# Kernel tuning notes

Hardware: AMD Instinct MI355X
Metric: run time of the kernel (lower is better)

Reference implementation:

```python
import jax, jax.numpy as jnp
import numpy as np

CAPACITY = 0.125


def setup_inputs() -> dict:
    key = jax.random.key(0)
    ks = jax.random.split(key, 6)
    b, s, d, dff = 4, 8192, 512, 2048
    x = jax.random.normal(ks[0], (b, s, d), dtype=jnp.float32)
    position_ids = jnp.tile(jnp.arange(s, dtype=jnp.int64)[None, :], (b, 1))
    Wr = jax.random.normal(ks[1], (d,), dtype=jnp.float32) * 0.02
    br = jnp.zeros((1,), dtype=jnp.float32)
    W1 = jax.random.normal(ks[2], (d, dff), dtype=jnp.float32) * 0.02
    b1 = jnp.zeros((dff,), dtype=jnp.float32)
    W2 = jax.random.normal(ks[3], (dff, d), dtype=jnp.float32) * 0.02
    b2 = jnp.zeros((d,), dtype=jnp.float32)
    return {"x": x, "position_ids": position_ids, "Wr": Wr, "br": br,
            "W1": W1, "b1": b1, "W2": W2, "b2": b2}


def reference(x, position_ids, Wr, br, W1, b1, W2, b2):
    b, s, d = x.shape
    # Router: Linear(d, 1) -> squeeze(-1)
    weights = jnp.einsum('bsd,d->bs', x, Wr) + br  # [b, s]
    k = int(CAPACITY * s)
    # Per-batch top-k threshold (k-th largest value)
    top_k_values = jax.lax.top_k(weights, k)[0]  # [b, k], sorted desc
    threshold = top_k_values[:, -1]              # [b]
    selected_mask = weights > threshold[:, None]  # strict >, ties excluded (matches torch)
    # Block: per-token MLP (Linear-GELU-Linear). Per-token ops commute with the
    # gather/scatter, so computing densely and masking is mathematically identical
    # to the original gather -> block -> weighted scatter.
    h = jax.nn.gelu(jnp.einsum('bsd,df->bsf', x, W1) + b1)
    y = jnp.einsum('bsf,fd->bsd', h, W2) + b2
    # processed_tokens (= block_out * router_weight on selected) + x on unselected
    out = jnp.where(selected_mask[..., None], y * weights[..., None], x)
    return out
```

## Files before the change

### kernel.cpp

```cpp
#include <hip/hip_runtime.h>
#include <hip/hip_bf16.h>

#define B_   4
#define S_   8192
#define D_   512
#define DFF_ 2048
#define K_TOP 1024
#define KS1  8
#define KS2  32
#define TILE_E (128*64)

typedef unsigned short u16;
typedef __attribute__((ext_vector_type(8))) short bf16x8;
typedef __attribute__((ext_vector_type(4))) float floatx4;

__device__ __forceinline__ unsigned f2key(float f){
    unsigned u = __float_as_uint(f);
    return (u & 0x80000000u) ? ~u : (u | 0x80000000u);
}
__device__ __forceinline__ u16 f2b(float f){
    unsigned u = __float_as_uint(f);
    u = (u + 0x7FFFu + ((u >> 16) & 1u)) >> 16;
    return (u16)u;
}
__device__ __forceinline__ float gelu_tanh(float v){
    float c = 0.7978845608028654f * (v + 0.044715f * v * v * v);
    return 0.5f * v * (1.0f + tanhf(c));
}
__device__ __forceinline__ void gl_lds16(const void* gptr, void* lptr){
    auto g = (const __attribute__((address_space(1))) unsigned int*)((uintptr_t)gptr);
    auto l = (__attribute__((address_space(3))) unsigned int*)((uintptr_t)lptr);
    __builtin_amdgcn_global_load_lds(g, l, 16, 0, 0);
}


__global__ __launch_bounds__(256) void wts_copy_kernel(
    const float4* __restrict__ x, float4* __restrict__ out,
    const float4* __restrict__ Wr4, const float* __restrict__ br,
    float* __restrict__ w_all, int* __restrict__ count)
{
    if (blockIdx.x == 0 && threadIdx.x == 0) *count = 0;
    const int wv = threadIdx.x >> 6, lane = threadIdx.x & 63;
    const int token = blockIdx.x * 4 + wv;
    const float4* xt = x + (size_t)token * 128;
    float acc = 0.f;
    #pragma unroll
    for (int i = 0; i < 2; i++){
        int j = lane + i * 64;
        float4 v = xt[j];
        out[(size_t)token * 128 + j] = v;
        float4 wvv = Wr4[j];
        acc += v.x*wvv.x + v.y*wvv.y + v.z*wvv.z + v.w*wvv.w;
    }
    #pragma unroll
    for (int off = 32; off > 0; off >>= 1) acc += __shfl_down(acc, off, 64);
    if (lane == 0) w_all[token] = acc + br[0];
}

__global__ __launch_bounds__(1024) void kth_compact_kernel(
    const float4* __restrict__ w_all4, int* __restrict__ count,
    int* __restrict__ idx)
{
    __shared__ unsigned keys[S_];
    __shared__ unsigned hist[16][256];
    __shared__ unsigned suffix[256];
    __shared__ unsigned sprefix;
    __shared__ int sremk;
    const int b = blockIdx.x, tid = threadIdx.x, wv = tid >> 6;
    const float4* row4 = w_all4 + (size_t)b * (S_ / 4);

    #pragma unroll
    for (int i = 0; i < 2; i++){
        int j = tid + i * 1024;
        float4 v = row4[j];
        keys[4*j+0] = f2key(v.x); keys[4*j+1] = f2key(v.y);
        keys[4*j+2] = f2key(v.z); keys[4*j+3] = f2key(v.w);
    }
    if (tid == 0){ sprefix = 0u; sremk = K_TOP; }
    __syncthreads();

    for (int pass = 3; pass >= 0; pass--){
        for (int i = tid; i < 16 * 256; i += 1024) ((unsigned*)hist)[i] = 0u;
        __syncthreads();
        const unsigned mask_hi = (pass == 3) ? 0u : (0xFFFFFFFFu << ((pass + 1) * 8));
        const unsigned pfx = sprefix;
        const int shift = pass * 8;
        #pragma unroll
        for (int i = 0; i < 8; i++){
            unsigned key = keys[tid + i * 1024];
            if ((key & mask_hi) == pfx)
                atomicAdd(&hist[wv][(key >> shift) & 255u], 1u);
        }
        __syncthreads();
        if (tid < 256){
            unsigned s = 0;
            #pragma unroll
            for (int h = 0; h < 16; h++) s += hist[h][tid];
            suffix[tid] = s;
        }
        __syncthreads();
        for (int off = 1; off < 256; off <<= 1){
            unsigned v = 0;
            if (tid < 256 && tid + off < 256) v = suffix[tid + off];
            __syncthreads();
            if (tid < 256) suffix[tid] += v;
            __syncthreads();
        }
        const int remk = sremk;
        __syncthreads();
        if (tid < 256){
            unsigned snext = (tid == 255) ? 0u : suffix[tid + 1];
            if (suffix[tid] >= (unsigned)remk && snext < (unsigned)remk){
                sprefix = pfx | ((unsigned)tid << shift);
                sremk = remk - (int)snext;
            }
        }
        __syncthreads();
    }

    const unsigned thr = sprefix;
    #pragma unroll
    for (int i = 0; i < 8; i++){
        int li = tid + i * 1024;
        if (keys[li] > thr){
            int p = atomicAdd(count, 1);
            idx[p] = b * S_ + li;
        }
    }
}

__global__ __launch_bounds__(256) void gather_kernel(
    const float* __restrict__ x, const int* __restrict__ idx,
    const int* __restrict__ countp, u16* __restrict__ XbT)
{
    const int mt = blockIdx.x, s = blockIdx.y;
    const int cnt = *countp;
    const int cl = threadIdx.x & 7, rb = threadIdx.x >> 3;
    #pragma unroll
    for (int it = 0; it < 4; it++){
        int r = rb + it * 32;
        int mg = mt * 128 + r;
        if (mg < cnt){
            const float* xp = x + (size_t)idx[mg] * D_ + s * 64 + cl * 8;
            float4 v0 = *(const float4*)xp;
            float4 v1 = *(const float4*)(xp + 4);
            bf16x8 bv;
            bv[0]=(short)f2b(v0.x); bv[1]=(short)f2b(v0.y);
            bv[2]=(short)f2b(v0.z); bv[3]=(short)f2b(v0.w);
            bv[4]=(short)f2b(v1.x); bv[5]=(short)f2b(v1.y);
            bv[6]=(short)f2b(v1.z); bv[7]=(short)f2b(v1.w);
            *(bf16x8*)&XbT[((size_t)(mt * KS1 + s) * 128 + r) * 64
                           + ((cl ^ (r & 7)) << 3)] = bv;
        }
    }
}

__global__ __launch_bounds__(256) void tconv_kernel(
    const float* __restrict__ src, u16* __restrict__ dst, int R, int C)
{
    __shared__ float tile[64][132];
    const int ct = blockIdx.x, s = blockIdx.y;
    const int tid = threadIdx.x;
    #pragma unroll
    for (int it = 0; it < 32; it++){
        int lin = it * 256 + tid;
        int kk = lin >> 7, nn = lin & 127;
        tile[kk][nn] = src[(size_t)(s * 64 + kk) * C + ct * 128 + nn];
    }
    __syncthreads();
    size_t base = ((size_t)(ct * (R / 64) + s)) * TILE_E;
    #pragma unroll
    for (int it = 0; it < 4; it++){
        int task = it * 256 + tid;
        int r = task >> 3, cl = task & 7;
        bf16x8 bv;
        #pragma unroll
        for (int e = 0; e < 8; e++) bv[e] = (short)f2b(tile[cl * 8 + e][r]);
        *(bf16x8*)&dst[base + (size_t)r * 64 + ((cl ^ (r & 7)) << 3)] = bv;
    }
}

__global__ __launch_bounds__(256) void ffn1_kernel(
    const u16* __restrict__ XbT, const u16* __restrict__ W1t,
    const int* __restrict__ countp, const float* __restrict__ bias1,
    u16* __restrict__ Ht)
{
    __shared__ __align__(16) u16 As[2][TILE_E];
    __shared__ __align__(16) u16 Bs[2][TILE_E];
    const int tid = threadIdx.x;
    const int cnt = *countp;
    const int mBlk = blockIdx.x, nBlk = blockIdx.y;
    const int lane = tid & 63, w = tid >> 6;
    const int wr = (w >> 1) * 64, wc = (w & 1) * 64;
    const int fr = lane & 15, quad = lane >> 4, fx = fr & 7;

    const char* Ag = (const char*)(XbT + (size_t)mBlk * KS1 * TILE_E) + tid * 16;
    const char* Bg = (const char*)(W1t + (size_t)nBlk * KS1 * TILE_E) + tid * 16;

    #pragma unroll
    for (int i = 0; i < 4; i++){
        gl_lds16(Ag + i*4096, (char*)As[0] + tid*16 + i*4096);
        gl_lds16(Bg + i*4096, (char*)Bs[0] + tid*16 + i*4096);
    }

    floatx4 acc[4][4] = {};
    for (int ksi = 0; ksi < KS1; ksi++){
        __syncthreads();
        if (ksi + 1 < KS1){
            const char* An = Ag + (size_t)(ksi+1) * 16384;
            const char* Bn = Bg + (size_t)(ksi+1) * 16384;
            char* Al = (char*)As[(ksi+1)&1] + tid*16;
            char* Bl = (char*)Bs[(ksi+1)&1] + tid*16;
            #pragma unroll
            for (int i = 0; i < 4; i++){
                gl_lds16(An + i*4096, Al + i*4096);
                gl_lds16(Bn + i*4096, Bl + i*4096);
            }
        }
        const u16* Ab = As[ksi&1];
        const u16* Bb = Bs[ksi&1];
        #pragma unroll
        for (int sub = 0; sub < 2; sub++){
            const int cch = ((sub*4 + quad) ^ fx) << 3;
            bf16x8 af[4], bf[4];
            #pragma unroll
            for (int i = 0; i < 4; i++) af[i] = *(const bf16x8*)&Ab[(wr + i*16 + fr)*64 + cch];
            #pragma unroll
            for (int j = 0; j < 4; j++) bf[j] = *(const bf16x8*)&Bb[(wc + j*16 + fr)*64 + cch];
            #pragma unroll
            for (int i = 0; i < 4; i++)
                #pragma unroll
                for (int j = 0; j < 4; j++)
                    acc[i][j] = __builtin_amdgcn_mfma_f32_16x16x32_bf16(af[i], bf[j], acc[i][j], 0, 0, 0);
        }
    }

    float bj[4];
    #pragma unroll
    for (int j = 0; j < 4; j++) bj[j] = bias1[nBlk*128 + wc + j*16 + fr];
    const int rbase = quad * 4;
    #pragma unroll
    for (int i = 0; i < 4; i++){
        #pragma unroll
        for (int rg = 0; rg < 4; rg++){
            int r128 = wr + i*16 + rbase + rg;
            int mg = mBlk*128 + r128;
            if (mg < cnt){
                #pragma unroll
                for (int j = 0; j < 4; j++){
                    int n = nBlk*128 + wc + j*16 + fr;
                    float v = gelu_tanh(acc[i][j][rg] + bj[j]);
                    Ht[((size_t)(mBlk * KS2 + (n >> 6)) * 128 + r128) * 64
                       + ((((n >> 3) & 7) ^ (r128 & 7)) << 3) + (n & 7)] = f2b(v);
                }
            }
        }
    }
}

__global__ __launch_bounds__(256) void ffn2_kernel(
    const u16* __restrict__ Ht, const u16* __restrict__ W2t,
    const int* __restrict__ countp, const int* __restrict__ idx,
    const float* __restrict__ w_all, const float* __restrict__ bias2,
    float* __restrict__ out)
{
    __shared__ __align__(16) u16 As[2][TILE_E];
    __shared__ __align__(16) u16 Bs[2][TILE_E];
    const int tid = threadIdx.x;
    const int cnt = *countp;
    const int mBlk = blockIdx.x, nBlk = blockIdx.y;
    const int lane = tid & 63, w = tid >> 6;
    const int wr = (w >> 1) * 64, wc = (w & 1) * 64;
    const int fr = lane & 15, quad = lane >> 4, fx = fr & 7;

    const char* Ag = (const char*)(Ht + (size_t)mBlk * KS2 * TILE_E) + tid * 16;
    const char* Bg = (const char*)(W2t + (size_t)nBlk * KS2 * TILE_E) + tid * 16;

    #pragma unroll
    for (int i = 0; i < 4; i++){
        gl_lds16(Ag + i*4096, (char*)As[0] + tid*16 + i*4096);
        gl_lds16(Bg + i*4096, (char*)Bs[0] + tid*16 + i*4096);
    }

    floatx4 acc[4][4] = {};
    for (int ksi = 0; ksi < KS2; ksi++){
        __syncthreads();
        if (ksi + 1 < KS2){
            const char* An = Ag + (size_t)(ksi+1) * 16384;
            const char* Bn = Bg + (size_t)(ksi+1) * 16384;
            char* Al = (char*)As[(ksi+1)&1] + tid*16;
            char* Bl = (char*)Bs[(ksi+1)&1] + tid*16;
            #pragma unroll
            for (int i = 0; i < 4; i++){
                gl_lds16(An + i*4096, Al + i*4096);
                gl_lds16(Bn + i*4096, Bl + i*4096);
            }
        }
        const u16* Ab = As[ksi&1];
        const u16* Bb = Bs[ksi&1];
        #pragma unroll
        for (int sub = 0; sub < 2; sub++){
            const int cch = ((sub*4 + quad) ^ fx) << 3;
            bf16x8 af[4], bf[4];
            #pragma unroll
            for (int i = 0; i < 4; i++) af[i] = *(const bf16x8*)&Ab[(wr + i*16 + fr)*64 + cch];
            #pragma unroll
            for (int j = 0; j < 4; j++) bf[j] = *(const bf16x8*)&Bb[(wc + j*16 + fr)*64 + cch];
            #pragma unroll
            for (int i = 0; i < 4; i++)
                #pragma unroll
                for (int j = 0; j < 4; j++)
                    acc[i][j] = __builtin_amdgcn_mfma_f32_16x16x32_bf16(af[i], bf[j], acc[i][j], 0, 0, 0);
        }
    }

    float bj[4];
    #pragma unroll
    for (int j = 0; j < 4; j++) bj[j] = bias2[nBlk*128 + wc + j*16 + fr];
    const int rbase = quad * 4;
    #pragma unroll
    for (int i = 0; i < 4; i++){
        #pragma unroll
        for (int rg = 0; rg < 4; rg++){
            int mg = mBlk*128 + wr + i*16 + rbase + rg;
            if (mg < cnt){
                int token = idx[mg];
                float wt = w_all[token];
                float* op = out + (size_t)token * D_;
                #pragma unroll
                for (int j = 0; j < 4; j++){
                    int n = nBlk*128 + wc + j*16 + fr;
                    op[n] = (acc[i][j][rg] + bj[j]) * wt;
                }
            }
        }
    }
}

extern "C" void kernel_launch(void* const* d_in, const int* in_sizes, int n_in,
                              void* d_out, int out_size, void* d_ws, size_t ws_size,
                              hipStream_t stream)
{
    const float* x  = (const float*)d_in[0];
    const float* Wr = (const float*)d_in[2];
    const float* br = (const float*)d_in[3];
    const float* W1 = (const float*)d_in[4];
    const float* b1 = (const float*)d_in[5];
    const float* W2 = (const float*)d_in[6];
    const float* b2 = (const float*)d_in[7];
    float* out = (float*)d_out;
    char* ws = (char*)d_ws;

    float* w_all = (float*)(ws + 0);
    int*   count = (int*)  (ws + 131088);
    int*   idx   = (int*)  (ws + 131104);
    u16*   XbT   = (u16*)  (ws + 262144);
    u16*   W1t   = (u16*)  (ws + 4456448);
    u16*   W2t   = (u16*)  (ws + 6553600);
    u16*   Ht    = (u16*)  (ws + 8650752);

    tconv_kernel<<<dim3(DFF_/128, D_/64),  256, 0, stream>>>(W1, W1t, D_, DFF_);
    tconv_kernel<<<dim3(D_/128,  DFF_/64), 256, 0, stream>>>(W2, W2t, DFF_, D_);
    wts_copy_kernel<<<(B_*S_)/4, 256, 0, stream>>>(
        (const float4*)x, (float4*)out, (const float4*)Wr, br, w_all, count);
    kth_compact_kernel<<<B_, 1024, 0, stream>>>((const float4*)w_all, count, idx);
    gather_kernel<<<dim3(32, KS1), 256, 0, stream>>>(x, idx, count, XbT);
    ffn1_kernel<<<dim3(32, DFF_/128), 256, 0, stream>>>(XbT, W1t, count, b1, Ht);
    ffn2_kernel<<<dim3(32, D_/128),   256, 0, stream>>>(Ht, W2t, count, idx, w_all, b2, out);
}
```

Before: 208.3 us.

## Widen K tiles to 128, stage GEMM epilogues through LDS, split ffn2 M tiles

```diff
diff --git a/kernel.cpp b/kernel.cpp
--- a/kernel.cpp
+++ b/kernel.cpp
@@ -6,9 +6,6 @@
 #define D_   512
 #define DFF_ 2048
 #define K_TOP 1024
-#define KS1  8
-#define KS2  32
-#define TILE_E (128*64)
 
 typedef unsigned short u16;
 typedef __attribute__((ext_vector_type(8))) short bf16x8;
@@ -23,9 +20,10 @@
     u = (u + 0x7FFFu + ((u >> 16) & 1u)) >> 16;
     return (u16)u;
 }
-__device__ __forceinline__ float gelu_tanh(float v){
-    float c = 0.7978845608028654f * (v + 0.044715f * v * v * v);
-    return 0.5f * v * (1.0f + tanhf(c));
+__device__ __forceinline__ float gelu_fast(float v){
+    float u = 1.5957691216f * v + 0.0713548162726f * v * v * v;
+    float e = __expf(u);
+    return v - v / (e + 1.0f);
 }
 __device__ __forceinline__ void gl_lds16(const void* gptr, void* lptr){
     auto g = (const __attribute__((address_space(1))) unsigned int*)((uintptr_t)gptr);
@@ -135,13 +133,14 @@
 {
     const int mt = blockIdx.x, s = blockIdx.y;
     const int cnt = *countp;
-    const int cl = threadIdx.x & 7, rb = threadIdx.x >> 3;
-    #pragma unroll
-    for (int it = 0; it < 4; it++){
-        int r = rb + it * 32;
+    const int cl = threadIdx.x & 15, r16 = threadIdx.x >> 4;
+    u16* base = XbT + (size_t)(mt * 4 + s) * 16384;
+    #pragma unroll
+    for (int it = 0; it < 8; it++){
+        int r = r16 + it * 16;
         int mg = mt * 128 + r;
         if (mg < cnt){
-            const float* xp = x + (size_t)idx[mg] * D_ + s * 64 + cl * 8;
+            const float* xp = x + (size_t)idx[mg] * D_ + s * 128 + cl * 8;
             float4 v0 = *(const float4*)xp;
             float4 v1 = *(const float4*)(xp + 4);
             bf16x8 bv;
@@ -149,8 +148,7 @@
             bv[2]=(short)f2b(v0.z); bv[3]=(short)f2b(v0.w);
             bv[4]=(short)f2b(v1.x); bv[5]=(short)f2b(v1.y);
             bv[6]=(short)f2b(v1.z); bv[7]=(short)f2b(v1.w);
-            *(bf16x8*)&XbT[((size_t)(mt * KS1 + s) * 128 + r) * 64
-                           + ((cl ^ (r & 7)) << 3)] = bv;
+            *(bf16x8*)&base[r * 128 + ((cl ^ (r & 15)) << 3)] = bv;
         }
     }
 }
@@ -158,25 +156,25 @@
 __global__ __launch_bounds__(256) void tconv_kernel(
     const float* __restrict__ src, u16* __restrict__ dst, int R, int C)
 {
-    __shared__ float tile[64][132];
-    const int ct = blockIdx.x, s = blockIdx.y;
+    __shared__ float tile[128][129];
+    const int ct = blockIdx.x, ks = blockIdx.y;
     const int tid = threadIdx.x;
     #pragma unroll
-    for (int it = 0; it < 32; it++){
+    for (int it = 0; it < 64; it++){
         int lin = it * 256 + tid;
         int kk = lin >> 7, nn = lin & 127;
-        tile[kk][nn] = src[(size_t)(s * 64 + kk) * C + ct * 128 + nn];
-    }
-    __syncthreads();
-    size_t base = ((size_t)(ct * (R / 64) + s)) * TILE_E;
-    #pragma unroll
-    for (int it = 0; it < 4; it++){
-        int task = it * 256 + tid;
-        int r = task >> 3, cl = task & 7;
+        tile[kk][nn] = src[(size_t)(ks * 128 + kk) * C + ct * 128 + nn];
+    }
+    __syncthreads();
+    u16* base = dst + (size_t)(ct * (R / 128) + ks) * 16384;
+    const int r = tid >> 1, h = tid & 1;
+    #pragma unroll
+    for (int c = 0; c < 8; c++){
+        int cl = h * 8 + c;
         bf16x8 bv;
         #pragma unroll
         for (int e = 0; e < 8; e++) bv[e] = (short)f2b(tile[cl * 8 + e][r]);
-        *(bf16x8*)&dst[base + (size_t)r * 64 + ((cl ^ (r & 7)) << 3)] = bv;
+        *(bf16x8*)&base[r * 128 + ((cl ^ (r & 15)) << 3)] = bv;
     }
 }
 
@@ -185,34 +183,34 @@
     const int* __restrict__ countp, const float* __restrict__ bias1,
     u16* __restrict__ Ht)
 {
-    __shared__ __align__(16) u16 As[2][TILE_E];
-    __shared__ __align__(16) u16 Bs[2][TILE_E];
+    __shared__ __align__(16) u16 As[2][16384];
+    __shared__ __align__(16) u16 Bs[2][16384];
     const int tid = threadIdx.x;
     const int cnt = *countp;
     const int mBlk = blockIdx.x, nBlk = blockIdx.y;
     const int lane = tid & 63, w = tid >> 6;
     const int wr = (w >> 1) * 64, wc = (w & 1) * 64;
-    const int fr = lane & 15, quad = lane >> 4, fx = fr & 7;
-
-    const char* Ag = (const char*)(XbT + (size_t)mBlk * KS1 * TILE_E) + tid * 16;
-    const char* Bg = (const char*)(W1t + (size_t)nBlk * KS1 * TILE_E) + tid * 16;
-
-    #pragma unroll
-    for (int i = 0; i < 4; i++){
+    const int fr = lane & 15, quad = lane >> 4;
+
+    const char* Ag = (const char*)(XbT + (size_t)mBlk * 4 * 16384) + tid * 16;
+    const char* Bg = (const char*)(W1t + (size_t)nBlk * 4 * 16384) + tid * 16;
+
+    #pragma unroll
+    for (int i = 0; i < 8; i++){
         gl_lds16(Ag + i*4096, (char*)As[0] + tid*16 + i*4096);
         gl_lds16(Bg + i*4096, (char*)Bs[0] + tid*16 + i*4096);
     }
 
     floatx4 acc[4][4] = {};
-    for (int ksi = 0; ksi < KS1; ksi++){
-        __syncthreads();
-        if (ksi + 1 < KS1){
-            const char* An = Ag + (size_t)(ksi+1) * 16384;
-            const char* Bn = Bg + (size_t)(ksi+1) * 16384;
+    for (int ksi = 0; ksi < 4; ksi++){
+        __syncthreads();
+        if (ksi + 1 < 4){
+            const char* An = Ag + (size_t)(ksi+1) * 32768;
+            const char* Bn = Bg + (size_t)(ksi+1) * 32768;
             char* Al = (char*)As[(ksi+1)&1] + tid*16;
             char* Bl = (char*)Bs[(ksi+1)&1] + tid*16;
             #pragma unroll
-            for (int i = 0; i < 4; i++){
+            for (int i = 0; i < 8; i++){
                 gl_lds16(An + i*4096, Al + i*4096);
                 gl_lds16(Bn + i*4096, Bl + i*4096);
             }
@@ -220,13 +218,18 @@
         const u16* Ab = As[ksi&1];
         const u16* Bb = Bs[ksi&1];
         #pragma unroll
-        for (int sub = 0; sub < 2; sub++){
-            const int cch = ((sub*4 + quad) ^ fx) << 3;
+        for (int ks2 = 0; ks2 < 4; ks2++){
             bf16x8 af[4], bf[4];
             #pragma unroll
-            for (int i = 0; i < 4; i++) af[i] = *(const bf16x8*)&Ab[(wr + i*16 + fr)*64 + cch];
-            #pragma unroll
-            for (int j = 0; j < 4; j++) bf[j] = *(const bf16x8*)&Bb[(wc + j*16 + fr)*64 + cch];
+            for (int i = 0; i < 4; i++){
+                int r = wr + i*16 + fr;
+                af[i] = *(const bf16x8*)&Ab[r*128 + (((ks2*4 + quad) ^ (r & 15)) << 3)];
+            }
+            #pragma unroll
+            for (int j = 0; j < 4; j++){
+                int r = wc + j*16 + fr;
+                bf[j] = *(const bf16x8*)&Bb[r*128 + (((ks2*4 + quad) ^ (r & 15)) << 3)];
+            }
             #pragma unroll
             for (int i = 0; i < 4; i++)
                 #pragma unroll
@@ -238,22 +241,31 @@
     float bj[4];
     #pragma unroll
     for (int j = 0; j < 4; j++) bj[j] = bias1[nBlk*128 + wc + j*16 + fr];
-    const int rbase = quad * 4;
+
+    __syncthreads();
+    u16* Cs = (u16*)As;
     #pragma unroll
     for (int i = 0; i < 4; i++){
         #pragma unroll
         for (int rg = 0; rg < 4; rg++){
-            int r128 = wr + i*16 + rbase + rg;
-            int mg = mBlk*128 + r128;
-            if (mg < cnt){
-                #pragma unroll
-                for (int j = 0; j < 4; j++){
-                    int n = nBlk*128 + wc + j*16 + fr;
-                    float v = gelu_tanh(acc[i][j][rg] + bj[j]);
-                    Ht[((size_t)(mBlk * KS2 + (n >> 6)) * 128 + r128) * 64
-                       + ((((n >> 3) & 7) ^ (r128 & 7)) << 3) + (n & 7)] = f2b(v);
-                }
-            }
+            int r = wr + i*16 + quad*4 + rg;
+            #pragma unroll
+            for (int j = 0; j < 4; j++){
+                int col = wc + j*16 + fr;
+                float v = gelu_fast(acc[i][j][rg] + bj[j]);
+                Cs[r*128 + ((((col >> 3) ^ (r & 15)) << 3) | (col & 7))] = f2b(v);
+            }
+        }
+    }
+    __syncthreads();
+    const int r = tid >> 1, h = tid & 1;
+    int mg = mBlk*128 + r;
+    if (mg < cnt){
+        u16* dstp = Ht + (((size_t)(mBlk*2 + (r >> 6)) * 16 + nBlk) * 64 + (r & 63)) * 128;
+        #pragma unroll
+        for (int p = 0; p < 8; p++){
+            int pc = h*8 + p;
+            *(bf16x8*)&dstp[pc << 3] = *(const bf16x8*)&Cs[r*128 + (pc << 3)];
         }
     }
 }
@@ -264,50 +276,53 @@
     const float* __restrict__ w_all, const float* __restrict__ bias2,
     float* __restrict__ out)
 {
-    __shared__ __align__(16) u16 As[2][TILE_E];
-    __shared__ __align__(16) u16 Bs[2][TILE_E];
+    __shared__ __align__(16) u16 As[2][8192];
+    __shared__ __align__(16) u16 Bs[2][16384];
     const int tid = threadIdx.x;
     const int cnt = *countp;
     const int mBlk = blockIdx.x, nBlk = blockIdx.y;
     const int lane = tid & 63, w = tid >> 6;
-    const int wr = (w >> 1) * 64, wc = (w & 1) * 64;
-    const int fr = lane & 15, quad = lane >> 4, fx = fr & 7;
-
-    const char* Ag = (const char*)(Ht + (size_t)mBlk * KS2 * TILE_E) + tid * 16;
-    const char* Bg = (const char*)(W2t + (size_t)nBlk * KS2 * TILE_E) + tid * 16;
-
-    #pragma unroll
-    for (int i = 0; i < 4; i++){
-        gl_lds16(Ag + i*4096, (char*)As[0] + tid*16 + i*4096);
-        gl_lds16(Bg + i*4096, (char*)Bs[0] + tid*16 + i*4096);
-    }
-
-    floatx4 acc[4][4] = {};
-    for (int ksi = 0; ksi < KS2; ksi++){
-        __syncthreads();
-        if (ksi + 1 < KS2){
+    const int wr = (w >> 1) * 32, wc = (w & 1) * 64;
+    const int fr = lane & 15, quad = lane >> 4;
+
+    const char* Ag = (const char*)(Ht + (size_t)mBlk * 16 * 8192) + tid * 16;
+    const char* Bg = (const char*)(W2t + (size_t)nBlk * 16 * 16384) + tid * 16;
+
+    #pragma unroll
+    for (int i = 0; i < 4; i++) gl_lds16(Ag + i*4096, (char*)As[0] + tid*16 + i*4096);
+    #pragma unroll
+    for (int i = 0; i < 8; i++) gl_lds16(Bg + i*4096, (char*)Bs[0] + tid*16 + i*4096);
+
+    floatx4 acc[2][4] = {};
+    for (int ksi = 0; ksi < 16; ksi++){
+        __syncthreads();
+        if (ksi + 1 < 16){
             const char* An = Ag + (size_t)(ksi+1) * 16384;
-            const char* Bn = Bg + (size_t)(ksi+1) * 16384;
+            const char* Bn = Bg + (size_t)(ksi+1) * 32768;
             char* Al = (char*)As[(ksi+1)&1] + tid*16;
             char* Bl = (char*)Bs[(ksi+1)&1] + tid*16;
             #pragma unroll
-            for (int i = 0; i < 4; i++){
-                gl_lds16(An + i*4096, Al + i*4096);
-                gl_lds16(Bn + i*4096, Bl + i*4096);
-            }
+            for (int i = 0; i < 4; i++) gl_lds16(An + i*4096, Al + i*4096);
+            #pragma unroll
+            for (int i = 0; i < 8; i++) gl_lds16(Bn + i*4096, Bl + i*4096);
         }
         const u16* Ab = As[ksi&1];
         const u16* Bb = Bs[ksi&1];
         #pragma unroll
-        for (int sub = 0; sub < 2; sub++){
-            const int cch = ((sub*4 + quad) ^ fx) << 3;
-            bf16x8 af[4], bf[4];
-            #pragma unroll
-            for (int i = 0; i < 4; i++) af[i] = *(const bf16x8*)&Ab[(wr + i*16 + fr)*64 + cch];
-            #pragma unroll
-            for (int j = 0; j < 4; j++) bf[j] = *(const bf16x8*)&Bb[(wc + j*16 + fr)*64 + cch];
-            #pragma unroll
-            for (int i = 0; i < 4; i++)
+        for (int ks2 = 0; ks2 < 4; ks2++){
+            bf16x8 af[2], bf[4];
+            #pragma unroll
+            for (int i = 0; i < 2; i++){
+                int r = wr + i*16 + fr;
+                af[i] = *(const bf16x8*)&Ab[r*128 + (((ks2*4 + quad) ^ (r & 15)) << 3)];
+            }
+            #pragma unroll
+            for (int j = 0; j < 4; j++){
+                int r = wc + j*16 + fr;
+                bf[j] = *(const bf16x8*)&Bb[r*128 + (((ks2*4 + quad) ^ (r & 15)) << 3)];
+            }
+            #pragma unroll
+            for (int i = 0; i < 2; i++)
                 #pragma unroll
                 for (int j = 0; j < 4; j++)
                     acc[i][j] = __builtin_amdgcn_mfma_f32_16x16x32_bf16(af[i], bf[j], acc[i][j], 0, 0, 0);
@@ -317,22 +332,32 @@
     float bj[4];
     #pragma unroll
     for (int j = 0; j < 4; j++) bj[j] = bias2[nBlk*128 + wc + j*16 + fr];
-    const int rbase = quad * 4;
-    #pragma unroll
-    for (int i = 0; i < 4; i++){
+
+    __syncthreads();
+    float* Cs = (float*)Bs;
+    #pragma unroll
+    for (int i = 0; i < 2; i++){
         #pragma unroll
         for (int rg = 0; rg < 4; rg++){
-            int mg = mBlk*128 + wr + i*16 + rbase + rg;
-            if (mg < cnt){
-                int token = idx[mg];
-                float wt = w_all[token];
-                float* op = out + (size_t)token * D_;
-                #pragma unroll
-                for (int j = 0; j < 4; j++){
-                    int n = nBlk*128 + wc + j*16 + fr;
-                    op[n] = (acc[i][j][rg] + bj[j]) * wt;
-                }
-            }
+            int r = wr + i*16 + quad*4 + rg;
+            #pragma unroll
+            for (int j = 0; j < 4; j++)
+                Cs[r*128 + wc + j*16 + fr] = acc[i][j][rg] + bj[j];
+        }
+    }
+    __syncthreads();
+    const int r = tid >> 2, q = tid & 3;
+    int mg = mBlk*64 + r;
+    if (mg < cnt){
+        int token = idx[mg];
+        float wt = w_all[token];
+        float* op = out + (size_t)token * D_ + nBlk*128 + q*32;
+        const float4* cp = (const float4*)&Cs[r*128 + q*32];
+        #pragma unroll
+        for (int p = 0; p < 8; p++){
+            float4 vv = cp[p];
+            vv.x *= wt; vv.y *= wt; vv.z *= wt; vv.w *= wt;
+            ((float4*)op)[p] = vv;
         }
     }
 }
@@ -359,12 +384,12 @@
     u16*   W2t   = (u16*)  (ws + 6553600);
     u16*   Ht    = (u16*)  (ws + 8650752);
 
-    tconv_kernel<<<dim3(DFF_/128, D_/64),  256, 0, stream>>>(W1, W1t, D_, DFF_);
-    tconv_kernel<<<dim3(D_/128,  DFF_/64), 256, 0, stream>>>(W2, W2t, DFF_, D_);
+    tconv_kernel<<<dim3(DFF_/128, D_/128),  256, 0, stream>>>(W1, W1t, D_, DFF_);
+    tconv_kernel<<<dim3(D_/128,  DFF_/128), 256, 0, stream>>>(W2, W2t, DFF_, D_);
     wts_copy_kernel<<<(B_*S_)/4, 256, 0, stream>>>(
         (const float4*)x, (float4*)out, (const float4*)Wr, br, w_all, count);
     kth_compact_kernel<<<B_, 1024, 0, stream>>>((const float4*)w_all, count, idx);
-    gather_kernel<<<dim3(32, KS1), 256, 0, stream>>>(x, idx, count, XbT);
+    gather_kernel<<<dim3(32, 4), 256, 0, stream>>>(x, idx, count, XbT);
     ffn1_kernel<<<dim3(32, DFF_/128), 256, 0, stream>>>(XbT, W1t, count, b1, Ht);
-    ffn2_kernel<<<dim3(32, D_/128),   256, 0, stream>>>(Ht, W2t, count, idx, w_all, b2, out);
-}
+    ffn2_kernel<<<dim3(64, D_/128),   256, 0, stream>>>(Ht, W2t, count, idx, w_all, b2, out);
+}
```

Result: no change. 206.0 us (-1.1%).
